# Optimization experiments

Hardware: AMD Instinct MI355X
Metric: run time of the kernel (lower is better)

The kernel has to match this reference:

```python
import jax, jax.numpy as jnp
import numpy as np

B, S, D = 2, 2048, 1024
H, DK, DV = 16, 64, 64


def setup_inputs() -> dict:
    key = jax.random.key(0)
    ks = jax.random.split(key, 9)
    s = 0.02
    return {
        "x": jax.random.normal(ks[0], (B, S, D), dtype=jnp.float32),
        "mask": jnp.zeros((B, S), dtype=bool),  # True = padded position
        "Wq": jax.random.normal(ks[1], (D, H * DK), dtype=jnp.float32) * s,
        "bq": jnp.zeros((H * DK,), dtype=jnp.float32),
        "Wk": jax.random.normal(ks[2], (D, H * DK), dtype=jnp.float32) * s,
        "bk": jnp.zeros((H * DK,), dtype=jnp.float32),
        "Wv": jax.random.normal(ks[3], (D, H * DV), dtype=jnp.float32) * s,
        "bv": jnp.zeros((H * DV,), dtype=jnp.float32),
        "Wo": jax.random.normal(ks[4], (H * DV, D), dtype=jnp.float32) * s,
        "bo": jnp.zeros((D,), dtype=jnp.float32),
    }


def reference(x, mask, Wq, bq, Wk, bk, Wv, bv, Wo, bo):
    Bx, Sx, _ = x.shape
    # projections -> [B, H, S, dk/dv]
    q = (x @ Wq + bq).reshape(Bx, Sx, H, DK).transpose(0, 2, 1, 3)
    k = (x @ Wk + bk).reshape(Bx, Sx, H, DK).transpose(0, 2, 1, 3)
    v = (x @ Wv + bv).reshape(Bx, Sx, H, DV).transpose(0, 2, 1, 3)
    # scaled QK^T: [B, H, Sq, Sk]
    scores = jnp.einsum("bhqd,bhkd->bhqk", q, k) / jnp.sqrt(jnp.float32(DK))
    neg_inf = jnp.float32(-jnp.inf)
    # padding mask: True masks out key positions
    scores = jnp.where(mask[:, None, None, :], neg_inf, scores)
    # causal mask
    causal = jnp.triu(jnp.ones((Sx, Sx), dtype=bool), k=1)
    scores = jnp.where(causal[None, None, :, :], neg_inf, scores)
    attn = jax.nn.softmax(scores, axis=-1)
    out = jnp.einsum("bhqk,bhkd->bhqd", attn, v)  # [B, H, S, dv]
    out = out.transpose(0, 2, 1, 3).reshape(Bx, Sx, H * DV)
    return out @ Wo + bo
```

## Files before the change

kernel.cpp:

```cpp
#include <hip/hip_runtime.h>
#include <stdint.h>

typedef __bf16 bf16_t;
typedef __bf16 bf16x8 __attribute__((ext_vector_type(8)));
typedef float f32x4 __attribute__((ext_vector_type(4)));

#define S_LEN 2048
#define D_MODEL 1024
#define NH 16
#define DKV 64
#define BATCH 2

#define QSCALE 0.1803368801111204f

__device__ __forceinline__ uint16_t f2bfu(float f) {
    union { float f; uint32_t u; } c; c.f = f;
    return (uint16_t)((c.u + 0x7fffu + ((c.u >> 16) & 1u)) >> 16);
}
__device__ __forceinline__ bf16_t f2bf(float f) {
    union { uint16_t s; bf16_t b; } o; o.s = f2bfu(f);
    return o.b;
}
__device__ __forceinline__ uint32_t pack2t(float lo, float hi) {
    union { float f; uint32_t u; } a, b; a.f = lo; b.f = hi;
    return (a.u >> 16) | (b.u & 0xFFFF0000u);
}
__device__ __forceinline__ void gld_lds16(const bf16_t* g, bf16_t* l) {
    __builtin_amdgcn_global_load_lds(
        (const __attribute__((address_space(1))) void*)g,
        (__attribute__((address_space(3))) void*)l, 16, 0, 0);
}

__global__ __launch_bounds__(256) void k_convert_x(const float* __restrict__ x,
                                                   bf16_t* __restrict__ xb, int n) {
    int i = (blockIdx.x * 256 + threadIdx.x) * 4;
    if (i < n) {
        float4 v = *(const float4*)(x + i);
        xb[i + 0] = f2bf(v.x);
        xb[i + 1] = f2bf(v.y);
        xb[i + 2] = f2bf(v.z);
        xb[i + 3] = f2bf(v.w);
    }
}

__global__ __launch_bounds__(256) void k_transpose4(
    const float* __restrict__ Wq, const float* __restrict__ Wk,
    const float* __restrict__ Wv, const float* __restrict__ Wo,
    bf16_t* __restrict__ WqkvT, bf16_t* __restrict__ WoT) {
    __shared__ float tile[64][65];
    int k0 = blockIdx.x * 64;
    int n0 = blockIdx.y * 64;
    const float* W; bf16_t* WT; int np, nw;
    if (n0 < 3072) {
        W = (n0 < 1024) ? Wq : (n0 < 2048) ? Wk : Wv;
        np = n0 & 1023; WT = WqkvT; nw = n0;
    } else {
        W = Wo; np = n0 - 3072; WT = WoT; nw = n0 - 3072;
    }
    int tx = threadIdx.x & 63, ty = threadIdx.x >> 6;
    #pragma unroll
    for (int r = ty; r < 64; r += 4)
        tile[r][tx] = W[(size_t)(k0 + r) * 1024 + np + tx];
    __syncthreads();
    #pragma unroll
    for (int r = ty; r < 64; r += 4)
        WT[(size_t)(nw + r) * 1024 + k0 + tx] = f2bf(tile[tx][r]);
}

#define BM 128
#define BN 128
#define BKK 64

__global__ __launch_bounds__(256) void k_gemm_qkv(
    const bf16_t* __restrict__ A, const bf16_t* __restrict__ BT, int K,
    const float* __restrict__ bias0, const float* __restrict__ bias1,
    const float* __restrict__ bias2,
    bf16_t* __restrict__ outQ, bf16_t* __restrict__ outK, bf16_t* __restrict__ outVt) {
    __shared__ __align__(16) bf16_t As[BM * BKK];
    __shared__ __align__(16) bf16_t Bs[BN * BKK];
    int m0 = blockIdx.x * BM;
    int n0 = blockIdx.y * BN;
    int t = threadIdx.x;
    int wid = t >> 6, lane = t & 63, l15 = lane & 15, quad = lane >> 4;
    int wr = (wid >> 1) * 64, wc = (wid & 1) * 64;
    int srow = t >> 3;
    int schunk = (t & 7) ^ (srow & 7);
    int sldst = (t & 7) * 8;
    const f32x4 fzero = {0.f, 0.f, 0.f, 0.f};
    f32x4 acc[4][4];
    #pragma unroll
    for (int i = 0; i < 4; i++)
        #pragma unroll
        for (int j = 0; j < 4; j++) acc[i][j] = fzero;

    int r7 = l15 & 7;
    for (int k0 = 0; k0 < K; k0 += BKK) {
        #pragma unroll
        for (int p = 0; p < 4; p++) {
            int r = p * 32 + srow;
            gld_lds16(&A[(size_t)(m0 + r) * K + k0 + schunk * 8], &As[r * 64 + sldst]);
            gld_lds16(&BT[(size_t)(n0 + r) * K + k0 + schunk * 8], &Bs[r * 64 + sldst]);
        }
        __syncthreads();
        #pragma unroll
        for (int kk = 0; kk < BKK; kk += 32) {
            int g = quad + (kk >> 3);
            int col = ((g ^ r7) << 3);
            bf16x8 af[4], bfr[4];
            #pragma unroll
            for (int mt = 0; mt < 4; mt++)
                af[mt] = *(const bf16x8*)&As[(wr + mt * 16 + l15) * 64 + col];
            #pragma unroll
            for (int nt = 0; nt < 4; nt++)
                bfr[nt] = *(const bf16x8*)&Bs[(wc + nt * 16 + l15) * 64 + col];
            #pragma unroll
            for (int mt = 0; mt < 4; mt++)
                #pragma unroll
                for (int nt = 0; nt < 4; nt++)
                    acc[mt][nt] = __builtin_amdgcn_mfma_f32_16x16x32_bf16(
                        af[mt], bfr[nt], acc[mt][nt], 0, 0, 0);
        }
        __syncthreads();
    }

    #pragma unroll
    for (int mt = 0; mt < 4; mt++) {
        #pragma unroll
        for (int nt = 0; nt < 4; nt++) {
            int gc = n0 + wc + nt * 16 + l15;
            int sec = gc >> 10;
            int nn = gc & 1023;
            int h = nn >> 6, d = nn & 63;
            int gr0 = m0 + wr + mt * 16 + quad * 4;
            int b = gr0 >> 11, s0 = gr0 & 2047;
            if (sec == 2) {
                float bv = bias2[nn];
                uint32_t lo = (uint32_t)f2bfu(acc[mt][nt][0] + bv) |
                              ((uint32_t)f2bfu(acc[mt][nt][1] + bv) << 16);
                uint32_t hi = (uint32_t)f2bfu(acc[mt][nt][2] + bv) |
                              ((uint32_t)f2bfu(acc[mt][nt][3] + bv) << 16);
                uint2 pk; pk.x = lo; pk.y = hi;
                *(uint2*)&outVt[(((size_t)(b * NH + h)) * DKV + d) * S_LEN + s0] = pk;
            } else {
                const float* bias = (sec == 0) ? bias0 : bias1;
                float bv = bias[nn];
                #pragma unroll
                for (int r = 0; r < 4; r++) {
                    float val = acc[mt][nt][r] + bv;
                    size_t idx = (((size_t)(b * NH + h)) * S_LEN + s0 + r) * DKV + d;
                    if (sec == 0) outQ[idx] = f2bf(val * QSCALE);
                    else          outK[idx] = f2bf(val);
                }
            }
        }
    }
}

__global__ __launch_bounds__(256) void k_gemm_out(
    const bf16_t* __restrict__ A, const bf16_t* __restrict__ BT, int N, int K,
    const float* __restrict__ bias, float* __restrict__ outF) {
    __shared__ __align__(16) bf16_t As[128 * 64];
    __shared__ __align__(16) bf16_t Bs[64 * 64];
    int m0 = blockIdx.x * 128;
    int n0 = blockIdx.y * 64;
    int t = threadIdx.x;
    int wid = t >> 6, lane = t & 63, l15 = lane & 15, quad = lane >> 4;
    int wr = wid * 32;
    int srow = t >> 3;
    int schunk = (t & 7) ^ (srow & 7);
    int sldst = (t & 7) * 8;
    const f32x4 fzero = {0.f, 0.f, 0.f, 0.f};
    f32x4 acc[2][4];
    #pragma unroll
    for (int i = 0; i < 2; i++)
        #pragma unroll
        for (int j = 0; j < 4; j++) acc[i][j] = fzero;

    int r7 = l15 & 7;
    for (int k0 = 0; k0 < K; k0 += 64) {
        #pragma unroll
        for (int p = 0; p < 4; p++) {
            int r = p * 32 + srow;
            gld_lds16(&A[(size_t)(m0 + r) * K + k0 + schunk * 8], &As[r * 64 + sldst]);
        }
        #pragma unroll
        for (int p = 0; p < 2; p++) {
            int r = p * 32 + srow;
            gld_lds16(&BT[(size_t)(n0 + r) * K + k0 + schunk * 8], &Bs[r * 64 + sldst]);
        }
        __syncthreads();
        #pragma unroll
        for (int kk = 0; kk < 64; kk += 32) {
            int g = quad + (kk >> 3);
            int col = ((g ^ r7) << 3);
            bf16x8 af[2], bfr[4];
            #pragma unroll
            for (int mt = 0; mt < 2; mt++)
                af[mt] = *(const bf16x8*)&As[(wr + mt * 16 + l15) * 64 + col];
            #pragma unroll
            for (int nt = 0; nt < 4; nt++)
                bfr[nt] = *(const bf16x8*)&Bs[(nt * 16 + l15) * 64 + col];
            #pragma unroll
            for (int mt = 0; mt < 2; mt++)
                #pragma unroll
                for (int nt = 0; nt < 4; nt++)
                    acc[mt][nt] = __builtin_amdgcn_mfma_f32_16x16x32_bf16(
                        af[mt], bfr[nt], acc[mt][nt], 0, 0, 0);
        }
        __syncthreads();
    }

    #pragma unroll
    for (int mt = 0; mt < 2; mt++) {
        #pragma unroll
        for (int nt = 0; nt < 4; nt++) {
            #pragma unroll
            for (int r = 0; r < 4; r++) {
                int gr = m0 + wr + mt * 16 + quad * 4 + r;
                int gc = n0 + nt * 16 + l15;
                outF[(size_t)gr * N + gc] = acc[mt][nt][r] + bias[gc];
            }
        }
    }
}

#define APD 72

__global__ __launch_bounds__(256) void k_attn6(
    const bf16_t* __restrict__ Q, const bf16_t* __restrict__ Kg,
    const bf16_t* __restrict__ Vt, const unsigned char* __restrict__ mask,
    bf16_t* __restrict__ O) {
    __shared__ __align__(16) char qps_raw[64 * APD * sizeof(bf16_t)];
    bf16_t (*Qs)[APD] = (bf16_t(*)[APD])qps_raw;
    bf16_t (*Ps)[16][APD] = (bf16_t(*)[16][APD])qps_raw;
    __shared__ __align__(16) bf16_t Ks[128 * 64];
    __shared__ __align__(16) bf16_t Vs[64 * 128];
    __shared__ float maskS[128];

    int bid = blockIdx.x;
    int bh = bid & 31;
    int qt = 31 - (bid >> 5);
    int b = bh >> 4, h = bh & 15;
    int t = threadIdx.x;
    int w = t >> 6, lane = t & 63, l15 = lane & 15, quad = lane >> 4;

    const bf16_t* Qbase = Q + ((size_t)bh * S_LEN + qt * 64) * DKV;
    {
        int r = t >> 3, c = (t & 7) * 8;
        *(uint4*)&Qs[r][c]      = *(const uint4*)&Qbase[(size_t)r * 64 + c];
        *(uint4*)&Qs[r + 32][c] = *(const uint4*)&Qbase[(size_t)(r + 32) * 64 + c];
    }
    __syncthreads();
    bf16x8 qf0 = *(const bf16x8*)&Qs[w * 16 + l15][quad * 8];
    bf16x8 qf1 = *(const bf16x8*)&Qs[w * 16 + l15][32 + quad * 8];

    const f32x4 fzero = {0.f, 0.f, 0.f, 0.f};
    f32x4 oacc[4];
    f32x4 lacc = fzero;
    #pragma unroll
    for (int nt = 0; nt < 4; nt++) oacc[nt] = fzero;

    const bf16_t one_b = (bf16_t)1.0f;
    const bf16x8 onesf = {one_b, one_b, one_b, one_b, one_b, one_b, one_b, one_b};

    int qg   = qt * 64 + w * 16 + l15;
    int qmin = qt * 64 + w * 16;
    int qmax = qmin + 15;
    int ktmax = qt >> 1;
    int r7 = l15 & 7;

    int srK = t >> 3;
    int scK = (t & 7) ^ (srK & 7);
    int slK = (t & 7) * 8;
    int srV = t >> 4;
    int scV = (t & 15) ^ (srV & 7);
    int slV = (t & 15) * 8;

    for (int kt = 0; kt <= ktmax; kt++) {
        __syncthreads();
        {
            const bf16_t* Kb = Kg + ((size_t)bh * S_LEN + kt * 128) * DKV;
            #pragma unroll
            for (int p = 0; p < 4; p++) {
                int r = p * 32 + srK;
                gld_lds16(&Kb[(size_t)r * 64 + scK * 8], &Ks[r * 64 + slK]);
            }
            #pragma unroll
            for (int p = 0; p < 4; p++) {
                int r = p * 16 + srV;
                gld_lds16(&Vt[((size_t)bh * DKV + r) * S_LEN + kt * 128 + scV * 8],
                          &Vs[r * 128 + slV]);
            }
        }
        if (t < 128) maskS[t] = mask[b * S_LEN + kt * 128 + t] ? -1e30f : 0.0f;
        __syncthreads();

        #pragma unroll
        for (int sub = 0; sub < 2; sub++) {
            int kbase = kt * 128 + sub * 64;
            if (kbase > qmax) break;

            f32x4 sacc[4];
            #pragma unroll
            for (int mt = 0; mt < 4; mt++) sacc[mt] = fzero;
            #pragma unroll
            for (int kk = 0; kk < 64; kk += 32) {
                bf16x8 qf = kk ? qf1 : qf0;
                int g = quad + (kk >> 3);
                int col = ((g ^ r7) << 3);
                #pragma unroll
                for (int mt = 0; mt < 4; mt++) {
                    bf16x8 af = *(const bf16x8*)&Ks[(sub * 64 + mt * 16 + l15) * 64 + col];
                    sacc[mt] = __builtin_amdgcn_mfma_f32_16x16x32_bf16(af, qf, sacc[mt], 0, 0, 0);
                }
            }

            bool diag = (kbase + 63 > qmin);
            #pragma unroll
            for (int mt = 0; mt < 4; mt++) {
                float4 m4 = *(const float4*)&maskS[sub * 64 + mt * 16 + quad * 4];
                #pragma unroll
                for (int r = 0; r < 4; r++)
                    sacc[mt][r] += ((const float*)&m4)[r];
                if (diag) {
                    int kgb = kbase + mt * 16 + quad * 4;
                    #pragma unroll
                    for (int r = 0; r < 4; r++)
                        if (kgb + r > qg) sacc[mt][r] = -1e30f;
                }
            }
            #pragma unroll
            for (int mt = 0; mt < 4; mt++) {
                uint32_t p0 = pack2t(exp2f(sacc[mt][0]), exp2f(sacc[mt][1]));
                uint32_t p1 = pack2t(exp2f(sacc[mt][2]), exp2f(sacc[mt][3]));
                union { uint32_t u[2]; uint2 v; } pk; pk.u[0] = p0; pk.u[1] = p1;
                *(uint2*)&Ps[w][l15][mt * 16 + quad * 4] = pk.v;
            }

            #pragma unroll
            for (int kk = 0; kk < 64; kk += 32) {
                bf16x8 pf = *(const bf16x8*)&Ps[w][l15][kk + quad * 8];
                int g2 = sub * 8 + (kk >> 3) + quad;
                int vcol = ((g2 ^ r7) << 3);
                #pragma unroll
                for (int nt = 0; nt < 4; nt++) {
                    bf16x8 vf = *(const bf16x8*)&Vs[(nt * 16 + l15) * 128 + vcol];
                    oacc[nt] = __builtin_amdgcn_mfma_f32_16x16x32_bf16(pf, vf, oacc[nt], 0, 0, 0);
                }
                lacc = __builtin_amdgcn_mfma_f32_16x16x32_bf16(pf, onesf, lacc, 0, 0, 0);
            }
        }
    }

    #pragma unroll
    for (int r = 0; r < 4; r++) {
        float l = lacc[r];
        float invl = l > 0.f ? 1.f / l : 0.f;
        int q = qt * 64 + w * 16 + quad * 4 + r;
        #pragma unroll
        for (int nt = 0; nt < 4; nt++) {
            int d = nt * 16 + l15;
            O[((size_t)b * S_LEN + q) * D_MODEL + h * DKV + d] = f2bf(oacc[nt][r] * invl);
        }
    }
}

extern "C" void kernel_launch(void* const* d_in, const int* in_sizes, int n_in,
                              void* d_out, int out_size, void* d_ws, size_t ws_size,
                              hipStream_t stream) {
    const float* x = (const float*)d_in[0];
    const unsigned char* mask = (const unsigned char*)d_in[1];
    const float* Wq = (const float*)d_in[2];
    const float* bq = (const float*)d_in[3];
    const float* Wk = (const float*)d_in[4];
    const float* bk = (const float*)d_in[5];
    const float* Wv = (const float*)d_in[6];
    const float* bv = (const float*)d_in[7];
    const float* Wo = (const float*)d_in[8];
    const float* bo = (const float*)d_in[9];
    float* out = (float*)d_out;

    char* ws = (char*)d_ws;
    const size_t MB = 1024 * 1024;
    bf16_t* xb    = (bf16_t*)(ws + 0 * MB);
    bf16_t* WqkvT = (bf16_t*)(ws + 8 * MB);
    bf16_t* WoT   = (bf16_t*)(ws + 14 * MB);
    bf16_t* Qb    = (bf16_t*)(ws + 16 * MB);
    bf16_t* Kb    = (bf16_t*)(ws + 24 * MB);
    bf16_t* Vtb   = (bf16_t*)(ws + 32 * MB);
    bf16_t* AOb   = (bf16_t*)(ws + 40 * MB);

    k_convert_x<<<dim3(4096), dim3(256), 0, stream>>>(x, xb, 4 * 1024 * 1024);
    k_transpose4<<<dim3(16, 64), dim3(256), 0, stream>>>(Wq, Wk, Wv, Wo, WqkvT, WoT);
    k_gemm_qkv<<<dim3(32, 24), dim3(256), 0, stream>>>(
        xb, WqkvT, 1024, bq, bk, bv, Qb, Kb, Vtb);
    k_attn6<<<dim3(1024), dim3(256), 0, stream>>>(Qb, Kb, Vtb, mask, AOb);
    k_gemm_out<<<dim3(32, 16), dim3(256), 0, stream>>>(
        AOb, WoT, 1024, 1024, bo, out);
}
```

Baseline: 191.1 us.

## Swizzle Q/P shared buffer, read mask from global, rebalance query-tile order

The attention kernel now keeps Q and P in one XOR-swizzled 64x64 shared buffer instead of a padded one. Mask bytes are read straight from global memory into registers, which removes the maskS staging store. Query tiles are assigned in a zigzag order so that heavy and light causal tiles interleave across the launch. pack2t now uses a single byte-permute, and the V epilogue reuses it. That means V is truncated to bf16 instead of rounded, which slightly changes precision.

```diff
diff --git a/kernel.cpp b/kernel.cpp
--- a/kernel.cpp
+++ b/kernel.cpp
@@ -23,7 +23,7 @@
 }
 __device__ __forceinline__ uint32_t pack2t(float lo, float hi) {
     union { float f; uint32_t u; } a, b; a.f = lo; b.f = hi;
-    return (a.u >> 16) | (b.u & 0xFFFF0000u);
+    return __builtin_amdgcn_perm(b.u, a.u, 0x07060302);
 }
 __device__ __forceinline__ void gld_lds16(const bf16_t* g, bf16_t* l) {
     __builtin_amdgcn_global_load_lds(
@@ -135,11 +135,9 @@
             int b = gr0 >> 11, s0 = gr0 & 2047;
             if (sec == 2) {
                 float bv = bias2[nn];
-                uint32_t lo = (uint32_t)f2bfu(acc[mt][nt][0] + bv) |
-                              ((uint32_t)f2bfu(acc[mt][nt][1] + bv) << 16);
-                uint32_t hi = (uint32_t)f2bfu(acc[mt][nt][2] + bv) |
-                              ((uint32_t)f2bfu(acc[mt][nt][3] + bv) << 16);
-                uint2 pk; pk.x = lo; pk.y = hi;
+                uint2 pk;
+                pk.x = pack2t(acc[mt][nt][0] + bv, acc[mt][nt][1] + bv);
+                pk.y = pack2t(acc[mt][nt][2] + bv, acc[mt][nt][3] + bv);
                 *(uint2*)&outVt[(((size_t)(b * NH + h)) * DKV + d) * S_LEN + s0] = pk;
             } else {
                 const float* bias = (sec == 0) ? bias0 : bias1;
@@ -224,35 +222,34 @@
     }
 }
 
-#define APD 72
-
-__global__ __launch_bounds__(256) void k_attn6(
+__global__ __launch_bounds__(256) void k_attn8(
     const bf16_t* __restrict__ Q, const bf16_t* __restrict__ Kg,
     const bf16_t* __restrict__ Vt, const unsigned char* __restrict__ mask,
     bf16_t* __restrict__ O) {
-    __shared__ __align__(16) char qps_raw[64 * APD * sizeof(bf16_t)];
-    bf16_t (*Qs)[APD] = (bf16_t(*)[APD])qps_raw;
-    bf16_t (*Ps)[16][APD] = (bf16_t(*)[16][APD])qps_raw;
+    __shared__ __align__(16) bf16_t QPs[64 * 64];
     __shared__ __align__(16) bf16_t Ks[128 * 64];
     __shared__ __align__(16) bf16_t Vs[64 * 128];
-    __shared__ float maskS[128];
 
     int bid = blockIdx.x;
     int bh = bid & 31;
-    int qt = 31 - (bid >> 5);
+    int u = bid >> 5;
+    int a = u & 7, g2 = u >> 3;
+    int qt = (g2 == 0) ? 31 - a : (g2 == 1) ? a : (g2 == 2) ? 23 - a : 8 + a;
     int b = bh >> 4, h = bh & 15;
     int t = threadIdx.x;
     int w = t >> 6, lane = t & 63, l15 = lane & 15, quad = lane >> 4;
+    int r7 = l15 & 7;
 
     const bf16_t* Qbase = Q + ((size_t)bh * S_LEN + qt * 64) * DKV;
     {
-        int r = t >> 3, c = (t & 7) * 8;
-        *(uint4*)&Qs[r][c]      = *(const uint4*)&Qbase[(size_t)r * 64 + c];
-        *(uint4*)&Qs[r + 32][c] = *(const uint4*)&Qbase[(size_t)(r + 32) * 64 + c];
+        int r = t >> 3, c8 = t & 7;
+        int sc = (c8 ^ (r & 7)) * 8;
+        *(uint4*)&QPs[r * 64 + sc]        = *(const uint4*)&Qbase[(size_t)r * 64 + c8 * 8];
+        *(uint4*)&QPs[(r + 32) * 64 + sc] = *(const uint4*)&Qbase[(size_t)(r + 32) * 64 + c8 * 8];
     }
     __syncthreads();
-    bf16x8 qf0 = *(const bf16x8*)&Qs[w * 16 + l15][quad * 8];
-    bf16x8 qf1 = *(const bf16x8*)&Qs[w * 16 + l15][32 + quad * 8];
+    bf16x8 qf0 = *(const bf16x8*)&QPs[(w * 16 + l15) * 64 + ((quad ^ r7) << 3)];
+    bf16x8 qf1 = *(const bf16x8*)&QPs[(w * 16 + l15) * 64 + (((4 + quad) ^ r7) << 3)];
 
     const f32x4 fzero = {0.f, 0.f, 0.f, 0.f};
     f32x4 oacc[4];
@@ -267,7 +264,6 @@
     int qmin = qt * 64 + w * 16;
     int qmax = qmin + 15;
     int ktmax = qt >> 1;
-    int r7 = l15 & 7;
 
     int srK = t >> 3;
     int scK = (t & 7) ^ (srK & 7);
@@ -292,7 +288,6 @@
                           &Vs[r * 128 + slV]);
             }
         }
-        if (t < 128) maskS[t] = mask[b * S_LEN + kt * 128 + t] ? -1e30f : 0.0f;
         __syncthreads();
 
         #pragma unroll
@@ -300,14 +295,18 @@
             int kbase = kt * 128 + sub * 64;
             if (kbase > qmax) break;
 
+            uint32_t mb[4];
+            #pragma unroll
+            for (int mt = 0; mt < 4; mt++)
+                mb[mt] = *(const uint32_t*)&mask[b * S_LEN + kbase + mt * 16 + quad * 4];
+
             f32x4 sacc[4];
             #pragma unroll
             for (int mt = 0; mt < 4; mt++) sacc[mt] = fzero;
             #pragma unroll
             for (int kk = 0; kk < 64; kk += 32) {
                 bf16x8 qf = kk ? qf1 : qf0;
-                int g = quad + (kk >> 3);
-                int col = ((g ^ r7) << 3);
+                int col = (((quad + (kk >> 3)) ^ r7) << 3);
                 #pragma unroll
                 for (int mt = 0; mt < 4; mt++) {
                     bf16x8 af = *(const bf16x8*)&Ks[(sub * 64 + mt * 16 + l15) * 64 + col];
@@ -318,10 +317,9 @@
             bool diag = (kbase + 63 > qmin);
             #pragma unroll
             for (int mt = 0; mt < 4; mt++) {
-                float4 m4 = *(const float4*)&maskS[sub * 64 + mt * 16 + quad * 4];
                 #pragma unroll
                 for (int r = 0; r < 4; r++)
-                    sacc[mt][r] += ((const float*)&m4)[r];
+                    sacc[mt][r] += (float)((mb[mt] >> (8 * r)) & 0xffu) * -1e30f;
                 if (diag) {
                     int kgb = kbase + mt * 16 + quad * 4;
                     #pragma unroll
@@ -331,17 +329,19 @@
             }
             #pragma unroll
             for (int mt = 0; mt < 4; mt++) {
-                uint32_t p0 = pack2t(exp2f(sacc[mt][0]), exp2f(sacc[mt][1]));
-                uint32_t p1 = pack2t(exp2f(sacc[mt][2]), exp2f(sacc[mt][3]));
-                union { uint32_t u[2]; uint2 v; } pk; pk.u[0] = p0; pk.u[1] = p1;
-                *(uint2*)&Ps[w][l15][mt * 16 + quad * 4] = pk.v;
+                uint2 pk;
+                pk.x = pack2t(exp2f(sacc[mt][0]), exp2f(sacc[mt][1]));
+                pk.y = pack2t(exp2f(sacc[mt][2]), exp2f(sacc[mt][3]));
+                int pc = (mt * 2 + (quad >> 1)) ^ r7;
+                *(uint2*)&QPs[(w * 16 + l15) * 64 + pc * 8 + (quad & 1) * 4] = pk;
             }
 
             #pragma unroll
             for (int kk = 0; kk < 64; kk += 32) {
-                bf16x8 pf = *(const bf16x8*)&Ps[w][l15][kk + quad * 8];
-                int g2 = sub * 8 + (kk >> 3) + quad;
-                int vcol = ((g2 ^ r7) << 3);
+                bf16x8 pf = *(const bf16x8*)&QPs[(w * 16 + l15) * 64 +
+                                                 (((quad + (kk >> 3)) ^ r7) << 3)];
+                int g2v = sub * 8 + (kk >> 3) + quad;
+                int vcol = ((g2v ^ r7) << 3);
                 #pragma unroll
                 for (int nt = 0; nt < 4; nt++) {
                     bf16x8 vf = *(const bf16x8*)&Vs[(nt * 16 + l15) * 128 + vcol];
@@ -394,7 +394,7 @@
     k_transpose4<<<dim3(16, 64), dim3(256), 0, stream>>>(Wq, Wk, Wv, Wo, WqkvT, WoT);
     k_gemm_qkv<<<dim3(32, 24), dim3(256), 0, stream>>>(
         xb, WqkvT, 1024, bq, bk, bv, Qb, Kb, Vtb);
-    k_attn6<<<dim3(1024), dim3(256), 0, stream>>>(Qb, Kb, Vtb, mask, AOb);
+    k_attn8<<<dim3(1024), dim3(256), 0, stream>>>(Qb, Kb, Vtb, mask, AOb);
     k_gemm_out<<<dim3(32, 16), dim3(256), 0, stream>>>(
         AOb, WoT, 1024, 1024, bo, out);
 }
```

Measured after the change: 190.8 us. About the same (-0.1%).
